# Optimization experiments

Hardware: AMD Instinct MI355X
Metric: run time of the kernel (lower is better)

The kernel has to match this reference:

```python
import jax, jax.numpy as jnp
import numpy as np

N_GRAPHS = 8
NODES_PER_G = 1024
EDGES_PER_G = 2048
N = N_GRAPHS * NODES_PER_G          # 8192 nodes
E = N_GRAPHS * EDGES_PER_G          # 16384 edges
IN_DIM, EDGE_DIM, HID, OUT_DIM, T = 10, 9, 64, 3, 5
EPS = 1e-6


def _lin(key, fan_in, fan_out):
    kw, kb = jax.random.split(key)
    s = 1.0 / np.sqrt(fan_in)
    return (jax.random.uniform(kw, (fan_in, fan_out), jnp.float32, -s, s),
            jax.random.uniform(kb, (fan_out,), jnp.float32, -s, s))


def setup_inputs() -> dict:
    key = jax.random.key(0)
    ks = jax.random.split(key, 32)
    x = jax.random.normal(ks[0], (N, IN_DIM), jnp.float32)
    edge_attr = jax.random.normal(ks[1], (E, EDGE_DIM), jnp.float32)
    # edges stay within their own graph (block structure)
    src_l = jax.random.randint(ks[2], (E,), 0, NODES_PER_G)
    dst_l = jax.random.randint(ks[3], (E,), 0, NODES_PER_G)
    off = jnp.repeat(jnp.arange(N_GRAPHS, dtype=jnp.int64) * NODES_PER_G, EDGES_PER_G)
    edge_index = jnp.stack([src_l.astype(jnp.int64) + off, dst_l.astype(jnp.int64) + off])
    batch = jnp.repeat(jnp.arange(N_GRAPHS, dtype=jnp.int64), NODES_PER_G)

    lift_w1, lift_b1 = _lin(ks[4], IN_DIM, HID)
    lift_w2, lift_b2 = _lin(ks[5], HID, HID)
    proj_w1, proj_b1 = _lin(ks[6], HID, HID)
    proj_w2, proj_b2 = _lin(ks[7], HID, OUT_DIM)

    def stackp(fn, base):
        ws, bs = zip(*[fn(ks[base + t]) for t in range(T)])
        return jnp.stack(ws), jnp.stack(bs)

    root_w, root_b = stackp(lambda k: _lin(k, HID, HID), 8)
    k_w1, k_b1 = stackp(lambda k: _lin(k, EDGE_DIM, HID), 13)
    k_w2, k_b2 = stackp(lambda k: _lin(k, HID, HID), 18)
    k_w3, k_b3 = stackp(lambda k: _lin(k, HID, HID * HID), 23)

    return dict(x=x, edge_attr=edge_attr,
                lift_w1=lift_w1, lift_b1=lift_b1, lift_w2=lift_w2, lift_b2=lift_b2,
                root_w=root_w, root_b=root_b,
                k_w1=k_w1, k_b1=k_b1, k_w2=k_w2, k_b2=k_b2, k_w3=k_w3, k_b3=k_b3,
                proj_w1=proj_w1, proj_b1=proj_b1, proj_w2=proj_w2, proj_b2=proj_b2,
                edge_index=edge_index, batch=batch)


def reference(x, edge_attr, lift_w1, lift_b1, lift_w2, lift_b2,
              root_w, root_b, k_w1, k_b1, k_w2, k_b2, k_w3, k_b3,
              proj_w1, proj_b1, proj_w2, proj_b2, edge_index, batch):
    src, dst = edge_index[0], edge_index[1]

    # --- per-graph edge_attr standardization (scatter mean/std over each graph's edges) ---
    eb = batch[src]                                           # graph id per edge [E]
    ones_e = jnp.ones((E,), jnp.float32)
    cnt = jax.ops.segment_sum(ones_e, eb, num_segments=N_GRAPHS)          # [G]
    mean = jax.ops.segment_sum(edge_attr, eb, num_segments=N_GRAPHS) / cnt[:, None]
    msq = jax.ops.segment_sum(edge_attr * edge_attr, eb, num_segments=N_GRAPHS) / cnt[:, None]
    std = jnp.sqrt(jnp.clip(msq - mean * mean, 0.0))
    ea = (edge_attr - mean[eb]) / (std[eb] + EPS)             # [E, edge_dim]

    # --- lift MLP ---
    v = jax.nn.relu(x @ lift_w1 + lift_b1) @ lift_w2 + lift_b2  # [N, HID]

    # --- T kernel layers: v' = relu(W_root v + mean_{j->i} K(e_ij) v_j) ---
    deg = jnp.clip(jax.ops.segment_sum(ones_e, dst, num_segments=N), 1.0)  # [N]
    for t in range(T):
        h = jax.nn.relu(ea @ k_w1[t] + k_b1[t])
        h = jax.nn.relu(h @ k_w2[t] + k_b2[t])
        ker = (h @ k_w3[t] + k_b3[t]).reshape(E, HID, HID)    # per-edge 64x64 kernel
        msg = jnp.einsum('eij,ej->ei', ker, v[src])           # [E, HID]
        aggr = jax.ops.segment_sum(msg, dst, num_segments=N) / deg[:, None]
        v = jax.nn.relu(v @ root_w[t] + root_b[t] + aggr)
        # dropout (p=0.1) is identity in eval mode

    # --- project MLP ---
    return jax.nn.relu(v @ proj_w1 + proj_b1) @ proj_w2 + proj_b2  # [N, OUT_DIM]
```

## Files before the change

### kernel.cpp

```cpp
#include <hip/hip_runtime.h>

#define N_GRAPHS    8
#define EDGES_PER_G 2048
#define NN          8192
#define EE          16384
#define IN_DIM      10
#define EDGE_DIM    9
#define HID         64
#define OUT_DIM     3
#define TT          5
#define EPSN        1e-6f

typedef float f32x4 __attribute__((ext_vector_type(4)));
typedef short bf16x8s __attribute__((ext_vector_type(8)));

union BF8 { __bf16 h[8]; bf16x8s v; };

__device__ inline void edgemlp_body_T(int e0, int tid,
    const float* __restrict__ ear, const float* __restrict__ meanb,
    const float* __restrict__ invstd,
    const float* __restrict__ w1, const float* __restrict__ b1,
    const float* __restrict__ w2, const float* __restrict__ b2,
    float (*sh)[HID], float (*st)[HID], float* __restrict__ h2T) {
  int g = tid >> 6, lane = tid & 63;
  int e = e0 + g;
  int gg = e >> 11;
  const float* er = ear + (size_t)e * EDGE_DIM;
  const float* mb = meanb + gg * EDGE_DIM;
  const float* is = invstd + gg * EDGE_DIM;
  float xn[EDGE_DIM];
#pragma unroll
  for (int d = 0; d < EDGE_DIM; ++d) xn[d] = (er[d] - mb[d]) * is[d];
  float a = b1[lane];
#pragma unroll
  for (int d = 0; d < EDGE_DIM; ++d) a += xn[d] * w1[d * HID + lane];
  sh[g][lane] = fmaxf(a, 0.f);
  __syncthreads();
  float o = b2[lane];
#pragma unroll
  for (int h = 0; h < HID; ++h) o += sh[g][h] * w2[h * HID + lane];
  st[g][lane] = fmaxf(o, 0.f);
  __syncthreads();
  int c = tid >> 2, eo = tid & 3;
  h2T[(size_t)c * EE + e0 + eo] = st[eo][c];
}

__global__ __launch_bounds__(256) void k_pre(
    const float* __restrict__ x,
    const float* __restrict__ lw1, const float* __restrict__ lb1,
    const float* __restrict__ lw2, const float* __restrict__ lb2,
    float* __restrict__ v,
    const float* __restrict__ kw3, const float* __restrict__ kb3,
    unsigned short* __restrict__ Bbf,
    const int* __restrict__ dst, float* __restrict__ degf,
    const float* __restrict__ ear, float* __restrict__ meanb,
    float* __restrict__ invstd, float* __restrict__ aggr) {
  __shared__ float sh[4][HID];
  int b = blockIdx.x;
  int g = threadIdx.x >> 6, lane = threadIdx.x & 63;
  if (b < NN / 4) {
    int n = b * 4 + g;
    const float* xr = x + n * IN_DIM;
    float a = lb1[lane];
#pragma unroll
    for (int d = 0; d < IN_DIM; ++d) a += xr[d] * lw1[d * HID + lane];
    sh[g][lane] = fmaxf(a, 0.f);
    __syncthreads();
    float o = lb2[lane];
#pragma unroll
    for (int h = 0; h < HID; ++h) o += sh[g][h] * lw2[h * HID + lane];
    v[n * HID + lane] = o;
  } else if (b < NN / 4 + 1024) {
    const int total = TT * 65 * 4096;
    for (int i = (b - NN / 4) * 256 + (int)threadIdx.x; i < total; i += 1024 * 256) {
      int xx   = i & 4095;
      int call = i >> 12;
      int t = call / 65;
      int c = call - t * 65;
      int sn = xx >> 9;
      int s  = sn >> 2, nt = sn & 3;
      int l9 = xx & 511;
      int ln = l9 >> 3, jj = l9 & 7;
      int nn15 = ln & 15, qq = ln >> 4;
      int x_in = (nt * 16 + nn15) * 64 + s * 32 + qq * 8 + jj;
      float val = (c < 64) ? kw3[(size_t)(t * 64 + c) * 4096 + x_in]
                           : kb3[(size_t)t * 4096 + x_in];
      union { __bf16 h; unsigned short s16; } u;
      u.h = (__bf16)val;
      Bbf[i] = u.s16;
    }
  } else if (b < NN / 4 + 1024 + EE / 256) {
    int e = (b - (NN / 4 + 1024)) * 256 + threadIdx.x;
    atomicAdd(&degf[dst[e]], 1.f);
  } else if (b < NN / 4 + 1024 + EE / 256 + N_GRAPHS) {
    int gg = b - (NN / 4 + 1024 + EE / 256);
    float ls[EDGE_DIM], lq[EDGE_DIM];
#pragma unroll
    for (int d = 0; d < EDGE_DIM; ++d) { ls[d] = 0.f; lq[d] = 0.f; }
    for (int e = threadIdx.x; e < EDGES_PER_G; e += blockDim.x) {
      const float* row = ear + (size_t)(gg * EDGES_PER_G + e) * EDGE_DIM;
#pragma unroll
      for (int d = 0; d < EDGE_DIM; ++d) { float xv = row[d]; ls[d] += xv; lq[d] += xv * xv; }
    }
#pragma unroll
    for (int d = 0; d < EDGE_DIM; ++d) {
#pragma unroll
      for (int off = 32; off > 0; off >>= 1) {
        ls[d] += __shfl_down(ls[d], off);
        lq[d] += __shfl_down(lq[d], off);
      }
    }
    if (lane == 0) {
#pragma unroll
      for (int d = 0; d < EDGE_DIM; ++d) {
        sh[g][d] = ls[d];
        sh[g][EDGE_DIM + d] = lq[d];
      }
    }
    __syncthreads();
    if (threadIdx.x < EDGE_DIM) {
      int d = threadIdx.x;
      float s0 = sh[0][d] + sh[1][d] + sh[2][d] + sh[3][d];
      float q0 = sh[0][EDGE_DIM + d] + sh[1][EDGE_DIM + d] +
                 sh[2][EDGE_DIM + d] + sh[3][EDGE_DIM + d];
      float m  = s0 * (1.0f / EDGES_PER_G);
      float mq = q0 * (1.0f / EDGES_PER_G);
      float var = fmaxf(mq - m * m, 0.f);
      meanb[gg * EDGE_DIM + d]  = m;
      invstd[gg * EDGE_DIM + d] = 1.f / (sqrtf(var) + EPSN);
    }
  } else {
    int idx = (b - (NN / 4 + 1024 + EE / 256 + N_GRAPHS)) * 256 + threadIdx.x;
    ((float4*)aggr)[idx] = make_float4(0.f, 0.f, 0.f, 0.f);
  }
}

__global__ __launch_bounds__(256) void k_em(const float* __restrict__ ear,
    const float* __restrict__ meanb, const float* __restrict__ invstd,
    const float* __restrict__ w1, const float* __restrict__ b1,
    const float* __restrict__ w2, const float* __restrict__ b2,
    float* __restrict__ h2T) {
  __shared__ float sh[4][HID];
  __shared__ float st[4][HID];
  edgemlp_body_T(blockIdx.x * 4, threadIdx.x, ear, meanb, invstd,
                 w1, b1, w2, b2, sh, st, h2T);
}

__global__ __launch_bounds__(256) void k_msg(const float* __restrict__ v,
    const float* __restrict__ h2T, const unsigned short* __restrict__ Bt,
    const int* __restrict__ src, const int* __restrict__ dst,
    float* __restrict__ aggr) {
  int kchunk = blockIdx.x & 3;
  int ebb    = (blockIdx.x >> 2) * 128;
  int w    = threadIdx.x >> 6;
  int lane = threadIdx.x & 63;
  int n15  = lane & 15;
  int q    = lane >> 4;
  int ebase = ebb + w * 32;

  bf16x8s ubf[2][2];
#pragma unroll
  for (int mt = 0; mt < 2; ++mt) {
    int e = ebase + mt * 16 + n15;
    const float4* vr = (const float4*)(v + (size_t)src[e] * HID);
    int f0 = q * 2;
#pragma unroll
    for (int s = 0; s < 2; ++s) {
      float4 pa = vr[s * 8 + f0], pb = vr[s * 8 + f0 + 1];
      BF8 u;
      u.h[0] = (__bf16)pa.x; u.h[1] = (__bf16)pa.y;
      u.h[2] = (__bf16)pa.z; u.h[3] = (__bf16)pa.w;
      u.h[4] = (__bf16)pb.x; u.h[5] = (__bf16)pb.y;
      u.h[6] = (__bf16)pb.z; u.h[7] = (__bf16)pb.w;
      ubf[mt][s] = u.v;
    }
  }

  f32x4 acc[2][4];
#pragma unroll
  for (int mt = 0; mt < 2; ++mt)
#pragma unroll
    for (int nt = 0; nt < 4; ++nt) acc[mt][nt] = (f32x4)0.0f;

  int c0 = kchunk * 16;
  const unsigned short* Bp = Bt + (size_t)c0 * 4096 + lane * 8;
  const float* hq = h2T + (size_t)c0 * EE + ebase + q * 4;

#pragma unroll 4
  for (int cc = 0; cc < 16; ++cc) {
    const unsigned short* Bc = Bp + (size_t)cc * 4096;
    bf16x8s bfr[2][4];
#pragma unroll
    for (int s = 0; s < 2; ++s)
#pragma unroll
      for (int nt = 0; nt < 4; ++nt)
        bfr[s][nt] = *(const bf16x8s*)(Bc + (s * 4 + nt) * 512);
    float4 h4[2];
    h4[0] = *(const float4*)(hq + (size_t)cc * EE);
    h4[1] = *(const float4*)(hq + (size_t)cc * EE + 16);
    f32x4 tmp[2][4];
#pragma unroll
    for (int mt = 0; mt < 2; ++mt)
#pragma unroll
      for (int nt = 0; nt < 4; ++nt) {
        f32x4 t0 = __builtin_amdgcn_mfma_f32_16x16x32_bf16(
            ubf[mt][0], bfr[0][nt], (f32x4)0.0f, 0, 0, 0);
        tmp[mt][nt] = __builtin_amdgcn_mfma_f32_16x16x32_bf16(
            ubf[mt][1], bfr[1][nt], t0, 0, 0, 0);
      }
#pragma unroll
    for (int mt = 0; mt < 2; ++mt) {
      float4 hh = h4[mt];
#pragma unroll
      for (int nt = 0; nt < 4; ++nt) {
        acc[mt][nt][0] += hh.x * tmp[mt][nt][0];
        acc[mt][nt][1] += hh.y * tmp[mt][nt][1];
        acc[mt][nt][2] += hh.z * tmp[mt][nt][2];
        acc[mt][nt][3] += hh.w * tmp[mt][nt][3];
      }
    }
  }

  if (kchunk == 3) {
    const unsigned short* Bc = Bt + (size_t)64 * 4096 + lane * 8;
    bf16x8s bfr[2][4];
#pragma unroll
    for (int s = 0; s < 2; ++s)
#pragma unroll
      for (int nt = 0; nt < 4; ++nt)
        bfr[s][nt] = *(const bf16x8s*)(Bc + (s * 4 + nt) * 512);
#pragma unroll
    for (int s = 0; s < 2; ++s)
#pragma unroll
      for (int mt = 0; mt < 2; ++mt)
#pragma unroll
        for (int nt = 0; nt < 4; ++nt)
          acc[mt][nt] = __builtin_amdgcn_mfma_f32_16x16x32_bf16(
              ubf[mt][s], bfr[s][nt], acc[mt][nt], 0, 0, 0);
  }

#pragma unroll
  for (int mt = 0; mt < 2; ++mt) {
#pragma unroll
    for (int r = 0; r < 4; ++r) {
      int e = ebase + mt * 16 + q * 4 + r;
      int d = dst[e];
      float* ag = aggr + (size_t)d * HID;
#pragma unroll
      for (int nt = 0; nt < 4; ++nt)
        atomicAdd(ag + nt * 16 + n15, acc[mt][nt][r]);
    }
  }
}

__global__ __launch_bounds__(256) void k_upd_em(
    float* __restrict__ v, const float* __restrict__ rw, const float* __restrict__ rb,
    float* __restrict__ aggr, const float* __restrict__ degf,
    const float* __restrict__ ear, const float* __restrict__ meanb,
    const float* __restrict__ invstd,
    const float* __restrict__ w1, const float* __restrict__ b1,
    const float* __restrict__ w2, const float* __restrict__ b2,
    float* __restrict__ h2T) {
  __shared__ float sh[4][HID];
  __shared__ float st[4][HID];
  int g = threadIdx.x >> 6, lane = threadIdx.x & 63;
  if (blockIdx.x < NN / 4) {
    int n = blockIdx.x * 4 + g;
    int idx = n * HID + lane;
    sh[g][lane] = v[idx];
    __syncthreads();
    float inv = 1.f / fmaxf(degf[n], 1.f);
    float o = rb[lane] + aggr[idx] * inv;
    aggr[idx] = 0.f;
#pragma unroll
    for (int h = 0; h < HID; ++h) o += sh[g][h] * rw[h * HID + lane];
    v[idx] = fmaxf(o, 0.f);
  } else {
    int e0 = (blockIdx.x - NN / 4) * 4;
    edgemlp_body_T(e0, threadIdx.x, ear, meanb, invstd,
                   w1, b1, w2, b2, sh, st, h2T);
  }
}

__global__ __launch_bounds__(256) void k_upd_proj(
    const float* __restrict__ v, const float* __restrict__ rw,
    const float* __restrict__ rb,
    const float* __restrict__ aggr, const float* __restrict__ degf,
    const float* __restrict__ pw1, const float* __restrict__ pb1,
    const float* __restrict__ pw2, const float* __restrict__ pb2,
    float* __restrict__ out) {
  __shared__ float sh[4][HID];
  int g = threadIdx.x >> 6, lane = threadIdx.x & 63;
  int n = blockIdx.x * 4 + g;
  int idx = n * HID + lane;
  sh[g][lane] = v[idx];
  __syncthreads();
  float inv = 1.f / fmaxf(degf[n], 1.f);
  float o = rb[lane] + aggr[idx] * inv;
#pragma unroll
  for (int h = 0; h < HID; ++h) o += sh[g][h] * rw[h * HID + lane];
  float vn = fmaxf(o, 0.f);
  __syncthreads();
  sh[g][lane] = vn;
  __syncthreads();
  float a = pb1[lane];
#pragma unroll
  for (int h = 0; h < HID; ++h) a += sh[g][h] * pw1[h * HID + lane];
  float h1 = fmaxf(a, 0.f);
  __syncthreads();
  sh[g][lane] = h1;
  __syncthreads();
  if (lane < OUT_DIM) {
    float oo = pb2[lane];
#pragma unroll
    for (int h = 0; h < HID; ++h) oo += sh[g][h] * pw2[h * OUT_DIM + lane];
    out[n * OUT_DIM + lane] = oo;
  }
}

extern "C" void kernel_launch(void* const* d_in, const int* in_sizes, int n_in,
                              void* d_out, int out_size, void* d_ws, size_t ws_size,
                              hipStream_t stream) {
  const float* x        = (const float*)d_in[0];
  const float* ear      = (const float*)d_in[1];
  const float* lift_w1  = (const float*)d_in[2];
  const float* lift_b1  = (const float*)d_in[3];
  const float* lift_w2  = (const float*)d_in[4];
  const float* lift_b2  = (const float*)d_in[5];
  const float* root_w   = (const float*)d_in[6];
  const float* root_b   = (const float*)d_in[7];
  const float* kw1      = (const float*)d_in[8];
  const float* kb1      = (const float*)d_in[9];
  const float* kw2      = (const float*)d_in[10];
  const float* kb2      = (const float*)d_in[11];
  const float* kw3      = (const float*)d_in[12];
  const float* kb3      = (const float*)d_in[13];
  const float* pw1      = (const float*)d_in[14];
  const float* pb1      = (const float*)d_in[15];
  const float* pw2      = (const float*)d_in[16];
  const float* pb2      = (const float*)d_in[17];
  const int* edge_index = (const int*)d_in[18];
  const int* src = edge_index;
  const int* dst = edge_index + EE;
  float* out = (float*)d_out;

  float* ws     = (float*)d_ws;
  float* aggr   = ws;
  float* degf   = aggr + NN * HID;
  float* h2T    = degf + NN;
  float* vbuf   = h2T + (size_t)HID * EE;
  float* meanb  = vbuf + NN * HID;
  float* invstd = meanb + 72;
  unsigned short* Bbf = (unsigned short*)(invstd + 72);

  hipMemsetAsync(degf, 0, NN * sizeof(float), stream);
  const int PRE_BLOCKS = NN / 4 + 1024 + EE / 256 + N_GRAPHS + NN * HID / 1024;
  k_pre<<<PRE_BLOCKS, 256, 0, stream>>>(
      x, lift_w1, lift_b1, lift_w2, lift_b2, vbuf, kw3, kb3, Bbf,
      dst, degf, ear, meanb, invstd, aggr);
  k_em<<<EE / 4, 256, 0, stream>>>(ear, meanb, invstd,
      kw1, kb1, kw2, kb2, h2T);

  for (int t = 0; t < TT; ++t) {
    k_msg<<<512, 256, 0, stream>>>(vbuf, h2T, Bbf + (size_t)t * 65 * 4096,
                                   src, dst, aggr);
    if (t < TT - 1) {
      int tt = t + 1;
      k_upd_em<<<NN / 4 + EE / 4, 256, 0, stream>>>(
          vbuf, root_w + (size_t)t * HID * HID, root_b + (size_t)t * HID,
          aggr, degf, ear, meanb, invstd,
          kw1 + (size_t)tt * EDGE_DIM * HID, kb1 + (size_t)tt * HID,
          kw2 + (size_t)tt * HID * HID, kb2 + (size_t)tt * HID, h2T);
    } else {
      k_upd_proj<<<NN / 4, 256, 0, stream>>>(
          vbuf, root_w + (size_t)t * HID * HID, root_b + (size_t)t * HID,
          aggr, degf, pw1, pb1, pw2, pb2, out);
    }
  }
}
```

Baseline: 395.8 us.

## Fuse next-layer edge MLP into message kernel with double-buffered h2T

Moves the edge MLP for layer t+1 into the message kernel's grid, using ping-pong h2T buffers so it can run alongside the layer-t message computation, and makes the update kernel node-only. The message kernel now gives each block 32 edges and splits the K chunks across its four waves, summing them in shared memory before one atomic per element. This cuts global atomics by about 4x. Stats and degree zeroing move to a small up-front kernel that replaces the memset, and the first edge MLP joins k_pre. In exchange the message kernel needs a large shared buffer (about 34KB per block), which can lower occupancy.

```diff
diff --git a/kernel.cpp b/kernel.cpp
--- a/kernel.cpp
+++ b/kernel.cpp
@@ -45,6 +45,55 @@
   h2T[(size_t)c * EE + e0 + eo] = st[eo][c];
 }
 
+__global__ __launch_bounds__(256) void k_stats(
+    const float* __restrict__ ear, float* __restrict__ meanb,
+    float* __restrict__ invstd, float* __restrict__ degf) {
+  __shared__ float sw[4][2 * EDGE_DIM];
+  int b = blockIdx.x;
+  int g = threadIdx.x >> 6, lane = threadIdx.x & 63;
+  if (b < N_GRAPHS) {
+    int gg = b;
+    float ls[EDGE_DIM], lq[EDGE_DIM];
+#pragma unroll
+    for (int d = 0; d < EDGE_DIM; ++d) { ls[d] = 0.f; lq[d] = 0.f; }
+    for (int e = threadIdx.x; e < EDGES_PER_G; e += blockDim.x) {
+      const float* row = ear + (size_t)(gg * EDGES_PER_G + e) * EDGE_DIM;
+#pragma unroll
+      for (int d = 0; d < EDGE_DIM; ++d) { float xv = row[d]; ls[d] += xv; lq[d] += xv * xv; }
+    }
+#pragma unroll
+    for (int d = 0; d < EDGE_DIM; ++d) {
+#pragma unroll
+      for (int off = 32; off > 0; off >>= 1) {
+        ls[d] += __shfl_down(ls[d], off);
+        lq[d] += __shfl_down(lq[d], off);
+      }
+    }
+    if (lane == 0) {
+#pragma unroll
+      for (int d = 0; d < EDGE_DIM; ++d) {
+        sw[g][d] = ls[d];
+        sw[g][EDGE_DIM + d] = lq[d];
+      }
+    }
+    __syncthreads();
+    if (threadIdx.x < EDGE_DIM) {
+      int d = threadIdx.x;
+      float s0 = sw[0][d] + sw[1][d] + sw[2][d] + sw[3][d];
+      float q0 = sw[0][EDGE_DIM + d] + sw[1][EDGE_DIM + d] +
+                 sw[2][EDGE_DIM + d] + sw[3][EDGE_DIM + d];
+      float m  = s0 * (1.0f / EDGES_PER_G);
+      float mq = q0 * (1.0f / EDGES_PER_G);
+      float var = fmaxf(mq - m * m, 0.f);
+      meanb[gg * EDGE_DIM + d]  = m;
+      invstd[gg * EDGE_DIM + d] = 1.f / (sqrtf(var) + EPSN);
+    }
+  } else {
+    int idx = (b - N_GRAPHS) * 256 + threadIdx.x;
+    ((float4*)degf)[idx] = make_float4(0.f, 0.f, 0.f, 0.f);
+  }
+}
+
 __global__ __launch_bounds__(256) void k_pre(
     const float* __restrict__ x,
     const float* __restrict__ lw1, const float* __restrict__ lb1,
@@ -53,13 +102,20 @@
     const float* __restrict__ kw3, const float* __restrict__ kb3,
     unsigned short* __restrict__ Bbf,
     const int* __restrict__ dst, float* __restrict__ degf,
-    const float* __restrict__ ear, float* __restrict__ meanb,
-    float* __restrict__ invstd, float* __restrict__ aggr) {
+    const float* __restrict__ ear, const float* __restrict__ meanb,
+    const float* __restrict__ invstd, float* __restrict__ aggr,
+    const float* __restrict__ w1, const float* __restrict__ b1,
+    const float* __restrict__ w2, const float* __restrict__ b2,
+    float* __restrict__ h2T0) {
   __shared__ float sh[4][HID];
+  __shared__ float st[4][HID];
   int b = blockIdx.x;
   int g = threadIdx.x >> 6, lane = threadIdx.x & 63;
-  if (b < NN / 4) {
-    int n = b * 4 + g;
+  if (b < EE / 4) {
+    edgemlp_body_T(b * 4, threadIdx.x, ear, meanb, invstd, w1, b1, w2, b2,
+                   sh, st, h2T0);
+  } else if (b < EE / 4 + NN / 4) {
+    int n = (b - EE / 4) * 4 + g;
     const float* xr = x + n * IN_DIM;
     float a = lb1[lane];
 #pragma unroll
@@ -70,9 +126,10 @@
 #pragma unroll
     for (int h = 0; h < HID; ++h) o += sh[g][h] * lw2[h * HID + lane];
     v[n * HID + lane] = o;
-  } else if (b < NN / 4 + 1024) {
+  } else if (b < EE / 4 + NN / 4 + 1024) {
     const int total = TT * 65 * 4096;
-    for (int i = (b - NN / 4) * 256 + (int)threadIdx.x; i < total; i += 1024 * 256) {
+    for (int i = (b - (EE / 4 + NN / 4)) * 256 + (int)threadIdx.x; i < total;
+         i += 1024 * 256) {
       int xx   = i & 4095;
       int call = i >> 12;
       int t = call / 65;
@@ -89,197 +146,151 @@
       u.h = (__bf16)val;
       Bbf[i] = u.s16;
     }
-  } else if (b < NN / 4 + 1024 + EE / 256) {
-    int e = (b - (NN / 4 + 1024)) * 256 + threadIdx.x;
+  } else if (b < EE / 4 + NN / 4 + 1024 + EE / 256) {
+    int e = (b - (EE / 4 + NN / 4 + 1024)) * 256 + threadIdx.x;
     atomicAdd(&degf[dst[e]], 1.f);
-  } else if (b < NN / 4 + 1024 + EE / 256 + N_GRAPHS) {
-    int gg = b - (NN / 4 + 1024 + EE / 256);
-    float ls[EDGE_DIM], lq[EDGE_DIM];
-#pragma unroll
-    for (int d = 0; d < EDGE_DIM; ++d) { ls[d] = 0.f; lq[d] = 0.f; }
-    for (int e = threadIdx.x; e < EDGES_PER_G; e += blockDim.x) {
-      const float* row = ear + (size_t)(gg * EDGES_PER_G + e) * EDGE_DIM;
-#pragma unroll
-      for (int d = 0; d < EDGE_DIM; ++d) { float xv = row[d]; ls[d] += xv; lq[d] += xv * xv; }
-    }
-#pragma unroll
-    for (int d = 0; d < EDGE_DIM; ++d) {
-#pragma unroll
-      for (int off = 32; off > 0; off >>= 1) {
-        ls[d] += __shfl_down(ls[d], off);
-        lq[d] += __shfl_down(lq[d], off);
-      }
-    }
-    if (lane == 0) {
-#pragma unroll
-      for (int d = 0; d < EDGE_DIM; ++d) {
-        sh[g][d] = ls[d];
-        sh[g][EDGE_DIM + d] = lq[d];
-      }
-    }
-    __syncthreads();
-    if (threadIdx.x < EDGE_DIM) {
-      int d = threadIdx.x;
-      float s0 = sh[0][d] + sh[1][d] + sh[2][d] + sh[3][d];
-      float q0 = sh[0][EDGE_DIM + d] + sh[1][EDGE_DIM + d] +
-                 sh[2][EDGE_DIM + d] + sh[3][EDGE_DIM + d];
-      float m  = s0 * (1.0f / EDGES_PER_G);
-      float mq = q0 * (1.0f / EDGES_PER_G);
-      float var = fmaxf(mq - m * m, 0.f);
-      meanb[gg * EDGE_DIM + d]  = m;
-      invstd[gg * EDGE_DIM + d] = 1.f / (sqrtf(var) + EPSN);
-    }
   } else {
-    int idx = (b - (NN / 4 + 1024 + EE / 256 + N_GRAPHS)) * 256 + threadIdx.x;
+    int idx = (b - (EE / 4 + NN / 4 + 1024 + EE / 256)) * 256 + threadIdx.x;
     ((float4*)aggr)[idx] = make_float4(0.f, 0.f, 0.f, 0.f);
   }
 }
 
-__global__ __launch_bounds__(256) void k_em(const float* __restrict__ ear,
-    const float* __restrict__ meanb, const float* __restrict__ invstd,
-    const float* __restrict__ w1, const float* __restrict__ b1,
-    const float* __restrict__ w2, const float* __restrict__ b2,
-    float* __restrict__ h2T) {
-  __shared__ float sh[4][HID];
-  __shared__ float st[4][HID];
-  edgemlp_body_T(blockIdx.x * 4, threadIdx.x, ear, meanb, invstd,
-                 w1, b1, w2, b2, sh, st, h2T);
-}
-
 __global__ __launch_bounds__(256) void k_msg(const float* __restrict__ v,
-    const float* __restrict__ h2T, const unsigned short* __restrict__ Bt,
+    const float* __restrict__ h2T_r, const unsigned short* __restrict__ Bt,
     const int* __restrict__ src, const int* __restrict__ dst,
-    float* __restrict__ aggr) {
-  int kchunk = blockIdx.x & 3;
-  int ebb    = (blockIdx.x >> 2) * 128;
-  int w    = threadIdx.x >> 6;
-  int lane = threadIdx.x & 63;
-  int n15  = lane & 15;
-  int q    = lane >> 4;
-  int ebase = ebb + w * 32;
-
-  bf16x8s ubf[2][2];
-#pragma unroll
-  for (int mt = 0; mt < 2; ++mt) {
-    int e = ebase + mt * 16 + n15;
-    const float4* vr = (const float4*)(v + (size_t)src[e] * HID);
-    int f0 = q * 2;
-#pragma unroll
-    for (int s = 0; s < 2; ++s) {
-      float4 pa = vr[s * 8 + f0], pb = vr[s * 8 + f0 + 1];
-      BF8 u;
-      u.h[0] = (__bf16)pa.x; u.h[1] = (__bf16)pa.y;
-      u.h[2] = (__bf16)pa.z; u.h[3] = (__bf16)pa.w;
-      u.h[4] = (__bf16)pb.x; u.h[5] = (__bf16)pb.y;
-      u.h[6] = (__bf16)pb.z; u.h[7] = (__bf16)pb.w;
-      ubf[mt][s] = u.v;
-    }
-  }
-
-  f32x4 acc[2][4];
-#pragma unroll
-  for (int mt = 0; mt < 2; ++mt)
-#pragma unroll
-    for (int nt = 0; nt < 4; ++nt) acc[mt][nt] = (f32x4)0.0f;
-
-  int c0 = kchunk * 16;
-  const unsigned short* Bp = Bt + (size_t)c0 * 4096 + lane * 8;
-  const float* hq = h2T + (size_t)c0 * EE + ebase + q * 4;
-
-#pragma unroll 4
-  for (int cc = 0; cc < 16; ++cc) {
-    const unsigned short* Bc = Bp + (size_t)cc * 4096;
-    bf16x8s bfr[2][4];
-#pragma unroll
-    for (int s = 0; s < 2; ++s)
-#pragma unroll
-      for (int nt = 0; nt < 4; ++nt)
-        bfr[s][nt] = *(const bf16x8s*)(Bc + (s * 4 + nt) * 512);
-    float4 h4[2];
-    h4[0] = *(const float4*)(hq + (size_t)cc * EE);
-    h4[1] = *(const float4*)(hq + (size_t)cc * EE + 16);
-    f32x4 tmp[2][4];
-#pragma unroll
-    for (int mt = 0; mt < 2; ++mt)
-#pragma unroll
-      for (int nt = 0; nt < 4; ++nt) {
-        f32x4 t0 = __builtin_amdgcn_mfma_f32_16x16x32_bf16(
-            ubf[mt][0], bfr[0][nt], (f32x4)0.0f, 0, 0, 0);
-        tmp[mt][nt] = __builtin_amdgcn_mfma_f32_16x16x32_bf16(
-            ubf[mt][1], bfr[1][nt], t0, 0, 0, 0);
-      }
-#pragma unroll
-    for (int mt = 0; mt < 2; ++mt) {
-      float4 hh = h4[mt];
-#pragma unroll
-      for (int nt = 0; nt < 4; ++nt) {
-        acc[mt][nt][0] += hh.x * tmp[mt][nt][0];
-        acc[mt][nt][1] += hh.y * tmp[mt][nt][1];
-        acc[mt][nt][2] += hh.z * tmp[mt][nt][2];
-        acc[mt][nt][3] += hh.w * tmp[mt][nt][3];
-      }
-    }
-  }
-
-  if (kchunk == 3) {
-    const unsigned short* Bc = Bt + (size_t)64 * 4096 + lane * 8;
-    bf16x8s bfr[2][4];
-#pragma unroll
-    for (int s = 0; s < 2; ++s)
-#pragma unroll
-      for (int nt = 0; nt < 4; ++nt)
-        bfr[s][nt] = *(const bf16x8s*)(Bc + (s * 4 + nt) * 512);
-#pragma unroll
-    for (int s = 0; s < 2; ++s)
-#pragma unroll
-      for (int mt = 0; mt < 2; ++mt)
-#pragma unroll
-        for (int nt = 0; nt < 4; ++nt)
-          acc[mt][nt] = __builtin_amdgcn_mfma_f32_16x16x32_bf16(
-              ubf[mt][s], bfr[s][nt], acc[mt][nt], 0, 0, 0);
-  }
-
-#pragma unroll
-  for (int mt = 0; mt < 2; ++mt) {
-#pragma unroll
-    for (int r = 0; r < 4; ++r) {
-      int e = ebase + mt * 16 + q * 4 + r;
-      int d = dst[e];
-      float* ag = aggr + (size_t)d * HID;
-#pragma unroll
-      for (int nt = 0; nt < 4; ++nt)
-        atomicAdd(ag + nt * 16 + n15, acc[mt][nt][r]);
-    }
-  }
-}
-
-__global__ __launch_bounds__(256) void k_upd_em(
-    float* __restrict__ v, const float* __restrict__ rw, const float* __restrict__ rb,
-    float* __restrict__ aggr, const float* __restrict__ degf,
+    float* __restrict__ aggr, int nEm,
     const float* __restrict__ ear, const float* __restrict__ meanb,
     const float* __restrict__ invstd,
     const float* __restrict__ w1, const float* __restrict__ b1,
     const float* __restrict__ w2, const float* __restrict__ b2,
-    float* __restrict__ h2T) {
+    float* __restrict__ h2T_w) {
+  __shared__ float red[4][32][68];
+  int b = blockIdx.x;
+  if (b < 512) {
+    int w    = threadIdx.x >> 6;
+    int lane = threadIdx.x & 63;
+    int n15  = lane & 15;
+    int q    = lane >> 4;
+    int ebase = b * 32;
+
+    bf16x8s ubf[2][2];
+#pragma unroll
+    for (int mt = 0; mt < 2; ++mt) {
+      int e = ebase + mt * 16 + n15;
+      const float4* vr = (const float4*)(v + (size_t)src[e] * HID);
+      int f0 = q * 2;
+#pragma unroll
+      for (int s = 0; s < 2; ++s) {
+        float4 pa = vr[s * 8 + f0], pb = vr[s * 8 + f0 + 1];
+        BF8 u;
+        u.h[0] = (__bf16)pa.x; u.h[1] = (__bf16)pa.y;
+        u.h[2] = (__bf16)pa.z; u.h[3] = (__bf16)pa.w;
+        u.h[4] = (__bf16)pb.x; u.h[5] = (__bf16)pb.y;
+        u.h[6] = (__bf16)pb.z; u.h[7] = (__bf16)pb.w;
+        ubf[mt][s] = u.v;
+      }
+    }
+
+    f32x4 acc[2][4];
+#pragma unroll
+    for (int mt = 0; mt < 2; ++mt)
+#pragma unroll
+      for (int nt = 0; nt < 4; ++nt) acc[mt][nt] = (f32x4)0.0f;
+
+    int c0 = w * 16;
+    const unsigned short* Bp = Bt + (size_t)c0 * 4096 + lane * 8;
+    const float* hq = h2T_r + (size_t)c0 * EE + ebase + q * 4;
+
+#pragma unroll 4
+    for (int cc = 0; cc < 16; ++cc) {
+      const unsigned short* Bc = Bp + (size_t)cc * 4096;
+      bf16x8s bfr[2][4];
+#pragma unroll
+      for (int s = 0; s < 2; ++s)
+#pragma unroll
+        for (int nt = 0; nt < 4; ++nt)
+          bfr[s][nt] = *(const bf16x8s*)(Bc + (s * 4 + nt) * 512);
+      float4 h4[2];
+      h4[0] = *(const float4*)(hq + (size_t)cc * EE);
+      h4[1] = *(const float4*)(hq + (size_t)cc * EE + 16);
+      f32x4 tmp[2][4];
+#pragma unroll
+      for (int mt = 0; mt < 2; ++mt)
+#pragma unroll
+        for (int nt = 0; nt < 4; ++nt) {
+          f32x4 t0 = __builtin_amdgcn_mfma_f32_16x16x32_bf16(
+              ubf[mt][0], bfr[0][nt], (f32x4)0.0f, 0, 0, 0);
+          tmp[mt][nt] = __builtin_amdgcn_mfma_f32_16x16x32_bf16(
+              ubf[mt][1], bfr[1][nt], t0, 0, 0, 0);
+        }
+#pragma unroll
+      for (int mt = 0; mt < 2; ++mt) {
+        float4 hh = h4[mt];
+#pragma unroll
+        for (int nt = 0; nt < 4; ++nt) {
+          acc[mt][nt][0] += hh.x * tmp[mt][nt][0];
+          acc[mt][nt][1] += hh.y * tmp[mt][nt][1];
+          acc[mt][nt][2] += hh.z * tmp[mt][nt][2];
+          acc[mt][nt][3] += hh.w * tmp[mt][nt][3];
+        }
+      }
+    }
+
+    if (w == 3) {
+      const unsigned short* Bc = Bt + (size_t)64 * 4096 + lane * 8;
+      bf16x8s bfr[2][4];
+#pragma unroll
+      for (int s = 0; s < 2; ++s)
+#pragma unroll
+        for (int nt = 0; nt < 4; ++nt)
+          bfr[s][nt] = *(const bf16x8s*)(Bc + (s * 4 + nt) * 512);
+#pragma unroll
+      for (int s = 0; s < 2; ++s)
+#pragma unroll
+        for (int mt = 0; mt < 2; ++mt)
+#pragma unroll
+          for (int nt = 0; nt < 4; ++nt)
+            acc[mt][nt] = __builtin_amdgcn_mfma_f32_16x16x32_bf16(
+                ubf[mt][s], bfr[s][nt], acc[mt][nt], 0, 0, 0);
+    }
+
+#pragma unroll
+    for (int mt = 0; mt < 2; ++mt)
+#pragma unroll
+      for (int nt = 0; nt < 4; ++nt)
+#pragma unroll
+        for (int r = 0; r < 4; ++r)
+          red[w][mt * 16 + q * 4 + r][nt * 16 + n15] = acc[mt][nt][r];
+    __syncthreads();
+
+    for (int i = threadIdx.x; i < 32 * HID; i += 256) {
+      int e = i >> 6, c = i & 63;
+      float s = red[0][e][c] + red[1][e][c] + red[2][e][c] + red[3][e][c];
+      atomicAdd(aggr + (size_t)dst[ebase + e] * HID + c, s);
+    }
+  } else if (b < 512 + nEm) {
+    float (*sh)[HID] = (float (*)[HID])&red[0][0][0];
+    float (*st)[HID] = (float (*)[HID])(&red[0][0][0] + 4 * HID);
+    edgemlp_body_T((b - 512) * 4, threadIdx.x, ear, meanb, invstd,
+                   w1, b1, w2, b2, sh, st, h2T_w);
+  }
+}
+
+__global__ __launch_bounds__(256) void k_upd(
+    float* __restrict__ v, const float* __restrict__ rw, const float* __restrict__ rb,
+    float* __restrict__ aggr, const float* __restrict__ degf) {
   __shared__ float sh[4][HID];
-  __shared__ float st[4][HID];
   int g = threadIdx.x >> 6, lane = threadIdx.x & 63;
-  if (blockIdx.x < NN / 4) {
-    int n = blockIdx.x * 4 + g;
-    int idx = n * HID + lane;
-    sh[g][lane] = v[idx];
-    __syncthreads();
-    float inv = 1.f / fmaxf(degf[n], 1.f);
-    float o = rb[lane] + aggr[idx] * inv;
-    aggr[idx] = 0.f;
-#pragma unroll
-    for (int h = 0; h < HID; ++h) o += sh[g][h] * rw[h * HID + lane];
-    v[idx] = fmaxf(o, 0.f);
-  } else {
-    int e0 = (blockIdx.x - NN / 4) * 4;
-    edgemlp_body_T(e0, threadIdx.x, ear, meanb, invstd,
-                   w1, b1, w2, b2, sh, st, h2T);
-  }
+  int n = blockIdx.x * 4 + g;
+  int idx = n * HID + lane;
+  sh[g][lane] = v[idx];
+  __syncthreads();
+  float inv = 1.f / fmaxf(degf[n], 1.f);
+  float o = rb[lane] + aggr[idx] * inv;
+  aggr[idx] = 0.f;
+#pragma unroll
+  for (int h = 0; h < HID; ++h) o += sh[g][h] * rw[h * HID + lane];
+  v[idx] = fmaxf(o, 0.f);
 }
 
 __global__ __launch_bounds__(256) void k_upd_proj(
@@ -347,30 +358,35 @@
   float* ws     = (float*)d_ws;
   float* aggr   = ws;
   float* degf   = aggr + NN * HID;
-  float* h2T    = degf + NN;
-  float* vbuf   = h2T + (size_t)HID * EE;
+  float* h2Ta   = degf + NN;
+  float* h2Tb   = h2Ta + (size_t)HID * EE;
+  float* vbuf   = h2Tb + (size_t)HID * EE;
   float* meanb  = vbuf + NN * HID;
   float* invstd = meanb + 72;
   unsigned short* Bbf = (unsigned short*)(invstd + 72);
 
-  hipMemsetAsync(degf, 0, NN * sizeof(float), stream);
-  const int PRE_BLOCKS = NN / 4 + 1024 + EE / 256 + N_GRAPHS + NN * HID / 1024;
+  k_stats<<<2 * N_GRAPHS, 256, 0, stream>>>(ear, meanb, invstd, degf);
+
+  const int PRE_BLOCKS = EE / 4 + NN / 4 + 1024 + EE / 256 + NN * HID / 1024;
   k_pre<<<PRE_BLOCKS, 256, 0, stream>>>(
       x, lift_w1, lift_b1, lift_w2, lift_b2, vbuf, kw3, kb3, Bbf,
-      dst, degf, ear, meanb, invstd, aggr);
-  k_em<<<EE / 4, 256, 0, stream>>>(ear, meanb, invstd,
-      kw1, kb1, kw2, kb2, h2T);
+      dst, degf, ear, meanb, invstd, aggr,
+      kw1, kb1, kw2, kb2, h2Ta);
 
   for (int t = 0; t < TT; ++t) {
-    k_msg<<<512, 256, 0, stream>>>(vbuf, h2T, Bbf + (size_t)t * 65 * 4096,
-                                   src, dst, aggr);
+    const float* hr = (t & 1) ? h2Tb : h2Ta;
+    float*       hw = (t & 1) ? h2Ta : h2Tb;
+    int nEm = (t < TT - 1) ? EE / 4 : 0;
+    int tt  = (t < TT - 1) ? t + 1 : t;
+    k_msg<<<512 + nEm, 256, 0, stream>>>(
+        vbuf, hr, Bbf + (size_t)t * 65 * 4096, src, dst, aggr, nEm,
+        ear, meanb, invstd,
+        kw1 + (size_t)tt * EDGE_DIM * HID, kb1 + (size_t)tt * HID,
+        kw2 + (size_t)tt * HID * HID, kb2 + (size_t)tt * HID, hw);
     if (t < TT - 1) {
-      int tt = t + 1;
-      k_upd_em<<<NN / 4 + EE / 4, 256, 0, stream>>>(
+      k_upd<<<NN / 4, 256, 0, stream>>>(
           vbuf, root_w + (size_t)t * HID * HID, root_b + (size_t)t * HID,
-          aggr, degf, ear, meanb, invstd,
-          kw1 + (size_t)tt * EDGE_DIM * HID, kb1 + (size_t)tt * HID,
-          kw2 + (size_t)tt * HID * HID, kb2 + (size_t)tt * HID, h2T);
+          aggr, degf);
     } else {
       k_upd_proj<<<NN / 4, 256, 0, stream>>>(
           vbuf, root_w + (size_t)t * HID * HID, root_b + (size_t)t * HID,
```

Measured after the change: 366.5 us. -7.4%, faster.
